# Kernel tuning notes

Hardware: AMD Instinct MI355X
Metric: run time of the kernel (lower is better)

## Reference

```python
import jax, jax.numpy as jnp
import numpy as np

B, N, F, E = 4, 4096, 64, 64
EPS = 1e-5  # torch LayerNorm default

def setup_inputs() -> dict:
    key = jax.random.key(0)
    k = jax.random.split(key, 5)
    x = jax.random.normal(k[0], (B, N, F), dtype=jnp.float32)
    # LayerNorm affine params
    ln_gamma = jnp.ones((F,), dtype=jnp.float32)
    ln_beta = jnp.zeros((F,), dtype=jnp.float32)
    # Stacked Linear(1, E) weights/biases: proj_w[i] == param_projectors[i].weight[:, 0]
    bound = 1.0  # kaiming_uniform for fan_in=1 -> U(-1, 1); bias U(-1, 1) as well
    proj_w = jax.random.uniform(k[1], (F, E), dtype=jnp.float32, minval=-bound, maxval=bound)
    proj_b = jax.random.uniform(k[2], (F, E), dtype=jnp.float32, minval=-bound, maxval=bound)
    param_embeddings = 0.02 * jax.random.normal(k[3], (F, E), dtype=jnp.float32)
    return {"x": x, "ln_gamma": ln_gamma, "ln_beta": ln_beta,
            "proj_w": proj_w, "proj_b": proj_b, "param_embeddings": param_embeddings}

def reference(x, ln_gamma, ln_beta, proj_w, proj_b, param_embeddings):
    # LayerNorm over last dim (feature_dim)
    mu = jnp.mean(x, axis=-1, keepdims=True)
    var = jnp.mean(jnp.square(x - mu), axis=-1, keepdims=True)
    xn = (x - mu) * jax.lax.rsqrt(var + EPS) * ln_gamma + ln_beta  # [B,N,F]
    # Per-feature scalar -> E projection fused: out[b,n,f,e] = xn[b,n,f]*w[f,e] + b[f,e] + emb[f,e]
    out = xn[..., None] * proj_w + (proj_b + param_embeddings)  # [B,N,F,E]
    Bs, Ns, Fs, Es = out.shape
    return out.reshape(Bs, Ns, Fs * Es)
```

## Files before the change

### kernel.cpp

```cpp
#include <hip/hip_runtime.h>

#define LN_EPS 1e-5f


typedef float f4 __attribute__((ext_vector_type(4)));

__global__ __launch_bounds__(256) void pte_kernel(
    const float* __restrict__ x,
    const float* __restrict__ gamma,
    const float* __restrict__ beta,
    const float* __restrict__ w,
    const float* __restrict__ pb,
    const float* __restrict__ emb,
    float* __restrict__ out)
{
    const int row  = blockIdx.x;
    const int tid  = threadIdx.x;
    const int lane = tid & 63;

    const f4* __restrict__ w4 = (const f4*)w;
    const f4* __restrict__ b4 = (const f4*)pb;
    const f4* __restrict__ e4 = (const f4*)emb;

    f4 wv[4], bv[4], ev[4];
    #pragma unroll
    for (int i = 0; i < 4; ++i) {
        int idx = i * 256 + tid;
        wv[i] = w4[idx];
        bv[i] = b4[idx];
        ev[i] = e4[idx];
    }

    float v  = x[(size_t)row * 64 + lane];
    float g  = gamma[lane];
    float bt = beta[lane];

    float s  = v;
    float s2 = v * v;
    #pragma unroll
    for (int m = 1; m < 64; m <<= 1) {
        s  += __shfl_xor(s,  m, 64);
        s2 += __shfl_xor(s2, m, 64);
    }
    float mu  = s * (1.0f / 64.0f);
    float var = fmaf(-mu, mu, s2 * (1.0f / 64.0f));
    float inv = rsqrtf(var + LN_EPS);
    float xn_lane = (v - mu) * inv * g + bt;

    const int fbase = ((tid >> 6) << 2) + (lane >> 4);

    f4* __restrict__ o4 = (f4*)(out + (size_t)row * 4096);
    #pragma unroll
    for (int i = 0; i < 4; ++i) {
        float xn = __shfl(xn_lane, i * 16 + fbase, 64);
        f4 r;
        r.x = fmaf(xn, wv[i].x, bv[i].x + ev[i].x);
        r.y = fmaf(xn, wv[i].y, bv[i].y + ev[i].y);
        r.z = fmaf(xn, wv[i].z, bv[i].z + ev[i].z);
        r.w = fmaf(xn, wv[i].w, bv[i].w + ev[i].w);
        __builtin_nontemporal_store(r, &o4[i * 256 + tid]);
    }
}

extern "C" void kernel_launch(void* const* d_in, const int* in_sizes, int n_in,
                              void* d_out, int out_size, void* d_ws, size_t ws_size,
                              hipStream_t stream) {
    const float* x     = (const float*)d_in[0];
    const float* gamma = (const float*)d_in[1];
    const float* beta  = (const float*)d_in[2];
    const float* w     = (const float*)d_in[3];
    const float* pb    = (const float*)d_in[4];
    const float* emb   = (const float*)d_in[5];
    float* out = (float*)d_out;

    const int rows = 4 * 4096;
    pte_kernel<<<rows, 256, 0, stream>>>(x, gamma, beta, w, pb, emb, out);
}
```

Baseline: 51.05 us.

## Split LayerNorm and projection emit into two kernels with workspace

```diff
diff --git a/kernel.cpp b/kernel.cpp
--- a/kernel.cpp
+++ b/kernel.cpp
@@ -5,38 +5,33 @@
 
 typedef float f4 __attribute__((ext_vector_type(4)));
 
-__global__ __launch_bounds__(256) void pte_kernel(
+__global__ __launch_bounds__(256) void pte_ln_kernel(
     const float* __restrict__ x,
     const float* __restrict__ gamma,
     const float* __restrict__ beta,
-    const float* __restrict__ w,
     const float* __restrict__ pb,
     const float* __restrict__ emb,
-    float* __restrict__ out)
+    float* __restrict__ xn_ws,
+    float* __restrict__ c_ws)
 {
-    const int row  = blockIdx.x;
     const int tid  = threadIdx.x;
     const int lane = tid & 63;
+    const int wave = tid >> 6;
+    const int row  = blockIdx.x * 4 + wave;
 
-    const f4* __restrict__ w4 = (const f4*)w;
-    const f4* __restrict__ b4 = (const f4*)pb;
-    const f4* __restrict__ e4 = (const f4*)emb;
-
-    f4 wv[4], bv[4], ev[4];
-    #pragma unroll
-    for (int i = 0; i < 4; ++i) {
-        int idx = i * 256 + tid;
-        wv[i] = w4[idx];
-        bv[i] = b4[idx];
-        ev[i] = e4[idx];
+    if (blockIdx.x == 0) {
+        const f4* __restrict__ b4 = (const f4*)pb;
+        const f4* __restrict__ e4 = (const f4*)emb;
+        f4* __restrict__ c4 = (f4*)c_ws;
+        #pragma unroll
+        for (int i = 0; i < 4; ++i) {
+            int idx = i * 256 + tid;
+            c4[idx] = b4[idx] + e4[idx];
+        }
     }
 
-    float v  = x[(size_t)row * 64 + lane];
-    float g  = gamma[lane];
-    float bt = beta[lane];
-
-    float s  = v;
-    float s2 = v * v;
+    float v = x[(size_t)row * 64 + lane];
+    float s = v, s2 = v * v;
     #pragma unroll
     for (int m = 1; m < 64; m <<= 1) {
         s  += __shfl_xor(s,  m, 64);
@@ -45,20 +40,40 @@
     float mu  = s * (1.0f / 64.0f);
     float var = fmaf(-mu, mu, s2 * (1.0f / 64.0f));
     float inv = rsqrtf(var + LN_EPS);
-    float xn_lane = (v - mu) * inv * g + bt;
+    xn_ws[(size_t)row * 64 + lane] = (v - mu) * inv * gamma[lane] + beta[lane];
+}
 
-    const int fbase = ((tid >> 6) << 2) + (lane >> 4);
+__global__ __launch_bounds__(256) void pte_emit_kernel(
+    const float* __restrict__ xn_ws,
+    const float* __restrict__ w,
+    const float* __restrict__ c_ws,
+    float* __restrict__ out)
+{
+    const int row = blockIdx.x;
+    const int tid = threadIdx.x;
 
+    const f4* __restrict__ w4 = (const f4*)w;
+    const f4* __restrict__ c4 = (const f4*)c_ws;
+    const float* __restrict__ xr = xn_ws + (size_t)row * 64;
     f4* __restrict__ o4 = (f4*)(out + (size_t)row * 4096);
+
+    const int f0 = tid >> 4;
+
+    float xn[4];
+    #pragma unroll
+    for (int i = 0; i < 4; ++i) xn[i] = xr[i * 16 + f0];
+
     #pragma unroll
     for (int i = 0; i < 4; ++i) {
-        float xn = __shfl(xn_lane, i * 16 + fbase, 64);
+        int idx = i * 256 + tid;
+        f4 wv = w4[idx];
+        f4 cv = c4[idx];
         f4 r;
-        r.x = fmaf(xn, wv[i].x, bv[i].x + ev[i].x);
-        r.y = fmaf(xn, wv[i].y, bv[i].y + ev[i].y);
-        r.z = fmaf(xn, wv[i].z, bv[i].z + ev[i].z);
-        r.w = fmaf(xn, wv[i].w, bv[i].w + ev[i].w);
-        __builtin_nontemporal_store(r, &o4[i * 256 + tid]);
+        r.x = fmaf(xn[i], wv.x, cv.x);
+        r.y = fmaf(xn[i], wv.y, cv.y);
+        r.z = fmaf(xn[i], wv.z, cv.z);
+        r.w = fmaf(xn[i], wv.w, cv.w);
+        __builtin_nontemporal_store(r, &o4[idx]);
     }
 }
 
@@ -74,5 +89,11 @@
     float* out = (float*)d_out;
 
     const int rows = 4 * 4096;
-    pte_kernel<<<rows, 256, 0, stream>>>(x, gamma, beta, w, pb, emb, out);
+
+    float* c_ws  = (float*)d_ws;
+    float* xn_ws = (float*)d_ws + 4096;
+
+    pte_ln_kernel<<<rows / 4, 256, 0, stream>>>(x, gamma, beta, pb, emb,
+                                                xn_ws, c_ws);
+    pte_emit_kernel<<<rows, 256, 0, stream>>>(xn_ws, w, c_ws, out);
 }
```

Result: slower. 56.35 us (+10.4%).
